# Optimization experiments

Hardware: AMD Instinct MI355X
Metric: run time of the kernel (lower is better)

Reference implementation:

```python
import jax, jax.numpy as jnp
import numpy as np

IN_DIMS = 1024
OUT_DIMS = 1024
N_TOKENS = 32768


def setup_inputs() -> dict:
    key = jax.random.key(0)
    k_x, k_wl0, k_wl1, k_scale, k_shift, k_noise = jax.random.split(key, 6)
    x = jax.random.normal(k_x, (N_TOKENS, IN_DIMS), dtype=jnp.float32)
    # weight_logits[..., 0]: magnitude logits, weight_logits[..., 1]: sign logits
    gain = np.sqrt(2.0)  # relu gain
    a = gain * np.sqrt(6.0 / (IN_DIMS + OUT_DIMS))
    mag_logits = jax.random.uniform(k_wl0, (OUT_DIMS, IN_DIMS), dtype=jnp.float32,
                                    minval=-a, maxval=a)  # logit(0.5)=0, so centered at 0
    sgn_logits = jax.random.uniform(k_wl1, (OUT_DIMS, IN_DIMS), dtype=jnp.float32,
                                    minval=-a, maxval=a)
    weight_logits = jnp.stack([mag_logits, sgn_logits], axis=-1)  # [O, I, 2]
    scale = jnp.full((OUT_DIMS,), np.float32(a), dtype=jnp.float32)
    shift = jnp.full((OUT_DIMS,), 0.01, dtype=jnp.float32)
    noise = jax.random.normal(k_noise, (N_TOKENS, OUT_DIMS), dtype=jnp.float32)
    return {"x": x, "weight_logits": weight_logits, "scale": scale,
            "shift": shift, "noise": noise}


def reference(x, weight_logits, scale, shift, noise):
    # train_forward of TernaryLinear
    weight_p = jax.nn.sigmoid(weight_logits)          # [O, I, 2]
    p_mag = weight_p[..., 0]                          # P(|w| = 1)
    p_sgn = weight_p[..., 1]                          # P(w > 0 | |w| = 1)
    s = 2.0 * p_sgn - 1.0
    weight_mean = p_mag * s                           # [O, I]
    weight_var = p_mag - (p_mag * p_mag) * (s * s)    # [O, I], >= 0
    out_mean = jnp.einsum('ni,oi->no', x, weight_mean)         # [N, O]
    out_var = jnp.einsum('ni,oi->no', x * x, weight_var)       # [N, O]
    out = out_mean + jnp.sqrt(out_var) * noise
    out = out * scale[None, :] + shift[None, :]
    return out
```

## Files before the change

### kernel.cpp

```cpp
#include <hip/hip_runtime.h>
#include <hip/hip_bf16.h>
#include <cmath>

#define N_TOK 32768
#define KDIM  1024
#define ODIM  1024

#define BM 128
#define BN 128
#define BK 64
#define NKT (KDIM / BK)
#define THREADS 512

typedef float          f32x4  __attribute__((ext_vector_type(4)));
typedef __bf16         bf16x8 __attribute__((ext_vector_type(8)));
typedef __bf16         bf16x4 __attribute__((ext_vector_type(4)));
typedef unsigned short us8    __attribute__((ext_vector_type(8)));
typedef unsigned short us2    __attribute__((ext_vector_type(2)));

static __device__ __forceinline__ unsigned short f2bf(float f) {
  unsigned u = __builtin_bit_cast(unsigned, f);
  u += 0x7FFFu + ((u >> 16) & 1u);
  return (unsigned short)(u >> 16);
}

static __device__ __forceinline__ f32x4 mfma16(us8 a, us8 b, f32x4 c) {
  return __builtin_amdgcn_mfma_f32_16x16x32_bf16(
      __builtin_bit_cast(bf16x8, a), __builtin_bit_cast(bf16x8, b), c, 0, 0, 0);
}

static __device__ __forceinline__ void gl_lds16(const void* g, void* l) {
  __builtin_amdgcn_global_load_lds(
      (const __attribute__((address_space(1))) void*)g,
      (__attribute__((address_space(3))) void*)l, 16, 0, 0);
}

__global__ void wprep_kernel(const float* __restrict__ wl,
                             unsigned short* __restrict__ wm,
                             unsigned short* __restrict__ wv) {
  int i = blockIdx.x * blockDim.x + threadIdx.x;
  f32x4 v = *reinterpret_cast<const f32x4*>(wl + (size_t)i * 4);
  float pm0 = 1.f / (1.f + expf(-v.x));
  float ps0 = 1.f / (1.f + expf(-v.y));
  float pm1 = 1.f / (1.f + expf(-v.z));
  float ps1 = 1.f / (1.f + expf(-v.w));
  float m0 = pm0 * (2.f * ps0 - 1.f);
  float m1 = pm1 * (2.f * ps1 - 1.f);
  float q0 = pm0 - m0 * m0;
  float q1 = pm1 - m1 * m1;
  us2 am = {f2bf(m0), f2bf(m1)};
  us2 av = {f2bf(q0), f2bf(q1)};
  *reinterpret_cast<us2*>(wm + (size_t)i * 2) = am;
  *reinterpret_cast<us2*>(wv + (size_t)i * 2) = av;
}

__global__ __launch_bounds__(THREADS, 4) void ternary_gemm(
    const float* __restrict__ x,
    const unsigned short* __restrict__ wm,
    const unsigned short* __restrict__ wv,
    const float* __restrict__ scale,
    const float* __restrict__ shift,
    const float* __restrict__ noise,
    float* __restrict__ out) {
  __shared__ alignas(16) char smem[67584];
  unsigned short* AsX  = (unsigned short*)smem;
  unsigned short* AsX2 = (unsigned short*)(smem + 16384);
  unsigned short* BsM  = (unsigned short*)(smem + 32768);
  unsigned short* BsV  = (unsigned short*)(smem + 49152);
  float* Mex = (float*)smem;
  float* Vex = ((float*)smem) + 4 * 32 * 66;

  const int tid  = threadIdx.x;
  const int lane = tid & 63;
  const int w    = tid >> 6;
  const bool isVar = (w >= 4);
  const int p    = w & 3;
  const int wr   = p >> 1;
  const int wc   = p & 1;
  const int l15  = lane & 15;
  const int l4   = lane >> 4;

  const int bid = blockIdx.x;
  const int swz = (bid & 7) * 256 + (bid >> 3);
  const int bm  = swz >> 3;
  const int bn  = swz & 7;
  const int rowBase = bm * BM;
  const int colBase = bn * BN;

  f32x4 acc[4][4];
#pragma unroll
  for (int i = 0; i < 4; ++i)
#pragma unroll
    for (int j = 0; j < 4; ++j) acc[i][j] = (f32x4)0.f;

  const float* xbase = x + (size_t)rowBase * KDIM;

  f32x4 apre[4];
#pragma unroll
  for (int jj = 0; jj < 4; ++jj) {
    int flat = jj * THREADS + tid;
    int r    = flat >> 4;
    int c4   = flat & 15;
    apre[jj] = *reinterpret_cast<const f32x4*>(xbase + (size_t)r * KDIM + c4 * 4);
  }

  const char* Abase = isVar ? (const char*)AsX2 : (const char*)AsX;
  const char* Bbase = isVar ? (const char*)BsV  : (const char*)BsM;

  for (int kt = 0; kt < NKT; ++kt) {
    const int k0 = kt * BK;

#pragma unroll
    for (int r = 0; r < 2; ++r) {
      int slot = r * THREADS + tid;
      int row  = slot >> 3;
      int j    = slot & 7;
      int ke   = (j ^ (row & 7)) << 3;
      size_t goff = (size_t)(colBase + row) * KDIM + k0 + ke;
      gl_lds16(wm + goff, (char*)BsM + slot * 16);
      gl_lds16(wv + goff, (char*)BsV + slot * 16);
    }

#pragma unroll
    for (int jj = 0; jj < 4; ++jj) {
      int flat = jj * THREADS + tid;
      int r    = flat >> 4;
      int c4   = flat & 15;
      f32x4 vx = apre[jj];
      bf16x4 bx  = {(__bf16)vx.x, (__bf16)vx.y, (__bf16)vx.z, (__bf16)vx.w};
      bf16x4 bx2 = {(__bf16)(vx.x * vx.x), (__bf16)(vx.y * vx.y),
                    (__bf16)(vx.z * vx.z), (__bf16)(vx.w * vx.w)};
      int off = r * 128 + ((c4 * 8) ^ ((r & 7) << 4));
      *reinterpret_cast<bf16x4*>((char*)AsX + off)  = bx;
      *reinterpret_cast<bf16x4*>((char*)AsX2 + off) = bx2;
    }

    __syncthreads();

    if (kt + 1 < NKT) {
      const float* xnext = xbase + (kt + 1) * BK;
#pragma unroll
      for (int jj = 0; jj < 4; ++jj) {
        int flat = jj * THREADS + tid;
        int r    = flat >> 4;
        int c4   = flat & 15;
        apre[jj] = *reinterpret_cast<const f32x4*>(xnext + (size_t)r * KDIM + c4 * 4);
      }
    }

#pragma unroll
    for (int ks = 0; ks < 2; ++ks) {
      us8 af[4], bf_[4];
      const int kb = ks * 64 + (l4 << 4);
#pragma unroll
      for (int am = 0; am < 4; ++am) {
        int row = wr * 64 + am * 16 + l15;
        int off = row * 128 + (kb ^ ((row & 7) << 4));
        af[am] = *reinterpret_cast<const us8*>(Abase + off);
      }
#pragma unroll
      for (int b = 0; b < 4; ++b) {
        int row = wc * 64 + b * 16 + l15;
        int off = row * 128 + (kb ^ ((row & 7) << 4));
        bf_[b] = *reinterpret_cast<const us8*>(Bbase + off);
      }
#pragma unroll
      for (int am = 0; am < 4; ++am)
#pragma unroll
        for (int b = 0; b < 4; ++b)
          acc[am][b] = mfma16(af[am], bf_[b], acc[am][b]);
    }
    __syncthreads();
  }

  if (!isVar) {
#pragma unroll
    for (int am = 2; am < 4; ++am)
#pragma unroll
      for (int b = 0; b < 4; ++b)
#pragma unroll
        for (int j = 0; j < 4; ++j) {
          int lr = am * 16 + l4 * 4 + j;
          int lc = b * 16 + l15;
          Mex[(p * 32 + (lr - 32)) * 66 + lc] = acc[am][b][j];
        }
  } else {
#pragma unroll
    for (int am = 0; am < 2; ++am)
#pragma unroll
      for (int b = 0; b < 4; ++b)
#pragma unroll
        for (int j = 0; j < 4; ++j) {
          int lr = am * 16 + l4 * 4 + j;
          int lc = b * 16 + l15;
          Vex[(p * 32 + lr) * 66 + lc] = acc[am][b][j];
        }
  }
  __syncthreads();

  if (!isVar) {
#pragma unroll
    for (int am = 0; am < 2; ++am)
#pragma unroll
      for (int b = 0; b < 4; ++b) {
        int col = colBase + wc * 64 + b * 16 + l15;
        float sc = scale[col];
        float sh = shift[col];
#pragma unroll
        for (int j = 0; j < 4; ++j) {
          int lr = am * 16 + l4 * 4 + j;
          float vv = Vex[(p * 32 + lr) * 66 + b * 16 + l15];
          size_t idx = (size_t)(rowBase + wr * 64 + lr) * ODIM + col;
          out[idx] = fmaf(acc[am][b][j] + sqrtf(fmaxf(vv, 0.f)) * noise[idx], sc, sh);
        }
      }
  } else {
#pragma unroll
    for (int am = 2; am < 4; ++am)
#pragma unroll
      for (int b = 0; b < 4; ++b) {
        int col = colBase + wc * 64 + b * 16 + l15;
        float sc = scale[col];
        float sh = shift[col];
#pragma unroll
        for (int j = 0; j < 4; ++j) {
          int lr = am * 16 + l4 * 4 + j;
          float mm = Mex[(p * 32 + (lr - 32)) * 66 + b * 16 + l15];
          size_t idx = (size_t)(rowBase + wr * 64 + lr) * ODIM + col;
          out[idx] = fmaf(mm + sqrtf(fmaxf(acc[am][b][j], 0.f)) * noise[idx], sc, sh);
        }
      }
  }
}

extern "C" void kernel_launch(void* const* d_in, const int* in_sizes, int n_in,
                              void* d_out, int out_size, void* d_ws, size_t ws_size,
                              hipStream_t stream) {
  const float* x     = (const float*)d_in[0];
  const float* wl    = (const float*)d_in[1];
  const float* scale = (const float*)d_in[2];
  const float* shift = (const float*)d_in[3];
  const float* noise = (const float*)d_in[4];
  float* out = (float*)d_out;

  unsigned short* wm = (unsigned short*)d_ws;
  unsigned short* wv = wm + (size_t)ODIM * KDIM;

  wprep_kernel<<<(ODIM * KDIM / 2) / 256, 256, 0, stream>>>(wl, wm, wv);

  ternary_gemm<<<(N_TOK / BM) * (ODIM / BN), THREADS, 0, stream>>>(
      x, wm, wv, scale, shift, noise, out);
}
```

Baseline: 207.9 us.

## Double-buffer LDS, enlarge row tile to 256, square x on the fly per warp

Moves the GEMM to a 256x128 tile with double-buffered LDS stages. The next k-tile's weight and x loads are issued before the current tile's MFMAs, and the bf16 x tile is written into the next buffer after compute, so only one barrier is needed per k-step. x is stored once in bf16, and the variance warps square it after reading it from LDS, instead of a second x² buffer being kept. This uses 128KB of LDS with occupancy 2, 128 accumulators per thread and extra ALU work in the variance warps, and it changes the epilogue exchange layout to an XOR swizzle.

```diff
diff --git a/kernel.cpp b/kernel.cpp
--- a/kernel.cpp
+++ b/kernel.cpp
@@ -6,17 +6,17 @@
 #define KDIM  1024
 #define ODIM  1024
 
-#define BM 128
+#define BM 256
 #define BN 128
 #define BK 64
 #define NKT (KDIM / BK)
 #define THREADS 512
+#define BUFSZ 65536
 
 typedef float          f32x4  __attribute__((ext_vector_type(4)));
 typedef __bf16         bf16x8 __attribute__((ext_vector_type(8)));
-typedef __bf16         bf16x4 __attribute__((ext_vector_type(4)));
 typedef unsigned short us8    __attribute__((ext_vector_type(8)));
-typedef unsigned short us2    __attribute__((ext_vector_type(2)));
+typedef unsigned short us2   __attribute__((ext_vector_type(2)));
 
 static __device__ __forceinline__ unsigned short f2bf(float f) {
   unsigned u = __builtin_bit_cast(unsigned, f);
@@ -24,6 +24,10 @@
   return (unsigned short)(u >> 16);
 }
 
+static __device__ __forceinline__ unsigned short bfc(float f) {
+  return __builtin_bit_cast(unsigned short, (__bf16)f);
+}
+
 static __device__ __forceinline__ f32x4 mfma16(us8 a, us8 b, f32x4 c) {
   return __builtin_amdgcn_mfma_f32_16x16x32_bf16(
       __builtin_bit_cast(bf16x8, a), __builtin_bit_cast(bf16x8, b), c, 0, 0, 0);
@@ -33,6 +37,16 @@
   __builtin_amdgcn_global_load_lds(
       (const __attribute__((address_space(1))) void*)g,
       (__attribute__((address_space(3))) void*)l, 16, 0, 0);
+}
+
+static __device__ __forceinline__ us8 sqr8(us8 a) {
+  us8 r;
+#pragma unroll
+  for (int i = 0; i < 8; ++i) {
+    float f = __builtin_bit_cast(float, (unsigned)a[i] << 16);
+    r[i] = bfc(f * f);
+  }
+  return r;
 }
 
 __global__ void wprep_kernel(const float* __restrict__ wl,
@@ -54,7 +68,7 @@
   *reinterpret_cast<us2*>(wv + (size_t)i * 2) = av;
 }
 
-__global__ __launch_bounds__(THREADS, 4) void ternary_gemm(
+__global__ __launch_bounds__(THREADS, 2) void ternary_gemm(
     const float* __restrict__ x,
     const unsigned short* __restrict__ wm,
     const unsigned short* __restrict__ wv,
@@ -62,13 +76,7 @@
     const float* __restrict__ shift,
     const float* __restrict__ noise,
     float* __restrict__ out) {
-  __shared__ alignas(16) char smem[67584];
-  unsigned short* AsX  = (unsigned short*)smem;
-  unsigned short* AsX2 = (unsigned short*)(smem + 16384);
-  unsigned short* BsM  = (unsigned short*)(smem + 32768);
-  unsigned short* BsV  = (unsigned short*)(smem + 49152);
-  float* Mex = (float*)smem;
-  float* Vex = ((float*)smem) + 4 * 32 * 66;
+  __shared__ alignas(16) char smem[2 * BUFSZ];
 
   const int tid  = threadIdx.x;
   const int lane = tid & 63;
@@ -81,153 +89,156 @@
   const int l4   = lane >> 4;
 
   const int bid = blockIdx.x;
-  const int swz = (bid & 7) * 256 + (bid >> 3);
+  const int swz = (bid & 7) * 128 + (bid >> 3);
   const int bm  = swz >> 3;
   const int bn  = swz & 7;
   const int rowBase = bm * BM;
   const int colBase = bn * BN;
 
-  f32x4 acc[4][4];
-#pragma unroll
-  for (int i = 0; i < 4; ++i)
+  f32x4 acc[8][4];
+#pragma unroll
+  for (int i = 0; i < 8; ++i)
 #pragma unroll
     for (int j = 0; j < 4; ++j) acc[i][j] = (f32x4)0.f;
 
-  const float* xbase = x + (size_t)rowBase * KDIM;
-
-  f32x4 apre[4];
-#pragma unroll
-  for (int jj = 0; jj < 4; ++jj) {
-    int flat = jj * THREADS + tid;
-    int r    = flat >> 4;
-    int c4   = flat & 15;
-    apre[jj] = *reinterpret_cast<const f32x4*>(xbase + (size_t)r * KDIM + c4 * 4);
-  }
-
-  const char* Abase = isVar ? (const char*)AsX2 : (const char*)AsX;
-  const char* Bbase = isVar ? (const char*)BsV  : (const char*)BsM;
+  const float* xb = x + (size_t)rowBase * KDIM;
+
+  auto stageB = [&](int kt, char* buf) {
+    const int k0 = kt * BK;
+    char* BsM = buf + 32768;
+    char* BsV = buf + 49152;
+#pragma unroll
+    for (int c = 0; c < 2; ++c) {
+      int flat = c * THREADS + tid;
+      int row  = flat >> 3;
+      int j    = flat & 7;
+      size_t goff = (size_t)(colBase + row) * KDIM + k0 + ((j ^ (row & 7)) << 3);
+      gl_lds16(wm + goff, BsM + flat * 16);
+      gl_lds16(wv + goff, BsV + flat * 16);
+    }
+  };
+  auto loadX = [&](int kt, f32x4* ap) {
+    const float* xt = xb + kt * BK;
+#pragma unroll
+    for (int c = 0; c < 4; ++c) {
+      int flat = c * THREADS + tid;
+      int row  = flat >> 3;
+      int j    = flat & 7;
+      const float* s = xt + (size_t)row * KDIM + j * 8;
+      ap[2 * c]     = *reinterpret_cast<const f32x4*>(s);
+      ap[2 * c + 1] = *reinterpret_cast<const f32x4*>(s + 4);
+    }
+  };
+  auto writeA = [&](const f32x4* ap, char* buf) {
+#pragma unroll
+    for (int c = 0; c < 4; ++c) {
+      int flat = c * THREADS + tid;
+      int row  = flat >> 3;
+      int j    = flat & 7;
+      f32x4 v0 = ap[2 * c], v1 = ap[2 * c + 1];
+      us8 o = {bfc(v0.x), bfc(v0.y), bfc(v0.z), bfc(v0.w),
+               bfc(v1.x), bfc(v1.y), bfc(v1.z), bfc(v1.w)};
+      int off = row * 128 + ((j * 16) ^ ((row & 7) << 4));
+      *reinterpret_cast<us8*>(buf + off) = o;
+    }
+  };
+
+  f32x4 ap[8];
+  stageB(0, smem);
+  loadX(0, ap);
+  writeA(ap, smem);
+  __syncthreads();
 
   for (int kt = 0; kt < NKT; ++kt) {
-    const int k0 = kt * BK;
-
-#pragma unroll
-    for (int r = 0; r < 2; ++r) {
-      int slot = r * THREADS + tid;
-      int row  = slot >> 3;
-      int j    = slot & 7;
-      int ke   = (j ^ (row & 7)) << 3;
-      size_t goff = (size_t)(colBase + row) * KDIM + k0 + ke;
-      gl_lds16(wm + goff, (char*)BsM + slot * 16);
-      gl_lds16(wv + goff, (char*)BsV + slot * 16);
-    }
-
-#pragma unroll
-    for (int jj = 0; jj < 4; ++jj) {
-      int flat = jj * THREADS + tid;
-      int r    = flat >> 4;
-      int c4   = flat & 15;
-      f32x4 vx = apre[jj];
-      bf16x4 bx  = {(__bf16)vx.x, (__bf16)vx.y, (__bf16)vx.z, (__bf16)vx.w};
-      bf16x4 bx2 = {(__bf16)(vx.x * vx.x), (__bf16)(vx.y * vx.y),
-                    (__bf16)(vx.z * vx.z), (__bf16)(vx.w * vx.w)};
-      int off = r * 128 + ((c4 * 8) ^ ((r & 7) << 4));
-      *reinterpret_cast<bf16x4*>((char*)AsX + off)  = bx;
-      *reinterpret_cast<bf16x4*>((char*)AsX2 + off) = bx2;
-    }
-
-    __syncthreads();
-
-    if (kt + 1 < NKT) {
-      const float* xnext = xbase + (kt + 1) * BK;
-#pragma unroll
-      for (int jj = 0; jj < 4; ++jj) {
-        int flat = jj * THREADS + tid;
-        int r    = flat >> 4;
-        int c4   = flat & 15;
-        apre[jj] = *reinterpret_cast<const f32x4*>(xnext + (size_t)r * KDIM + c4 * 4);
-      }
-    }
-
+    const char* cur = smem + (size_t)(kt & 1) * BUFSZ;
+    char*       nxt = smem + (size_t)((kt + 1) & 1) * BUFSZ;
+
+    if (kt + 1 < NKT) { stageB(kt + 1, nxt); loadX(kt + 1, ap); }
+
+    const char* Ab = cur;
+    const char* Bb = cur + 32768 + (isVar ? 16384 : 0);
 #pragma unroll
     for (int ks = 0; ks < 2; ++ks) {
-      us8 af[4], bf_[4];
       const int kb = ks * 64 + (l4 << 4);
-#pragma unroll
-      for (int am = 0; am < 4; ++am) {
-        int row = wr * 64 + am * 16 + l15;
-        int off = row * 128 + (kb ^ ((row & 7) << 4));
-        af[am] = *reinterpret_cast<const us8*>(Abase + off);
-      }
+      us8 bf_[4], af[8];
 #pragma unroll
       for (int b = 0; b < 4; ++b) {
         int row = wc * 64 + b * 16 + l15;
-        int off = row * 128 + (kb ^ ((row & 7) << 4));
-        bf_[b] = *reinterpret_cast<const us8*>(Bbase + off);
-      }
-#pragma unroll
-      for (int am = 0; am < 4; ++am)
+        bf_[b] = *reinterpret_cast<const us8*>(Bb + row * 128 + (kb ^ ((row & 7) << 4)));
+      }
+#pragma unroll
+      for (int i = 0; i < 8; ++i) {
+        int row = wr * 128 + i * 16 + l15;
+        af[i] = *reinterpret_cast<const us8*>(Ab + row * 128 + (kb ^ ((row & 7) << 4)));
+        if (isVar) af[i] = sqr8(af[i]);
+      }
+#pragma unroll
+      for (int i = 0; i < 8; ++i)
 #pragma unroll
         for (int b = 0; b < 4; ++b)
-          acc[am][b] = mfma16(af[am], bf_[b], acc[am][b]);
-    }
+          acc[i][b] = mfma16(af[i], bf_[b], acc[i][b]);
+    }
+
+    if (kt + 1 < NKT) writeA(ap, nxt);
+
     __syncthreads();
   }
 
+  float* Mx = (float*)smem;
+  float* Vx = (float*)(smem + 65536);
   if (!isVar) {
 #pragma unroll
-    for (int am = 2; am < 4; ++am)
+    for (int i = 4; i < 8; ++i)
 #pragma unroll
       for (int b = 0; b < 4; ++b)
 #pragma unroll
         for (int j = 0; j < 4; ++j) {
-          int lr = am * 16 + l4 * 4 + j;
+          int lr = (i - 4) * 16 + l4 * 4 + j;
           int lc = b * 16 + l15;
-          Mex[(p * 32 + (lr - 32)) * 66 + lc] = acc[am][b][j];
+          Mx[(p * 64 + lr) * 64 + (lc ^ ((lr & 4) << 2))] = acc[i][b][j];
         }
   } else {
 #pragma unroll
-    for (int am = 0; am < 2; ++am)
+    for (int i = 0; i < 4; ++i)
 #pragma unroll
       for (int b = 0; b < 4; ++b)
 #pragma unroll
         for (int j = 0; j < 4; ++j) {
-          int lr = am * 16 + l4 * 4 + j;
+          int lr = i * 16 + l4 * 4 + j;
           int lc = b * 16 + l15;
-          Vex[(p * 32 + lr) * 66 + lc] = acc[am][b][j];
+          Vx[(p * 64 + lr) * 64 + (lc ^ ((lr & 4) << 2))] = acc[i][b][j];
         }
   }
   __syncthreads();
 
   if (!isVar) {
 #pragma unroll
-    for (int am = 0; am < 2; ++am)
+    for (int i = 0; i < 4; ++i)
 #pragma unroll
       for (int b = 0; b < 4; ++b) {
         int col = colBase + wc * 64 + b * 16 + l15;
-        float sc = scale[col];
-        float sh = shift[col];
-#pragma unroll
-        for (int j = 0; j < 4; ++j) {
-          int lr = am * 16 + l4 * 4 + j;
-          float vv = Vex[(p * 32 + lr) * 66 + b * 16 + l15];
-          size_t idx = (size_t)(rowBase + wr * 64 + lr) * ODIM + col;
-          out[idx] = fmaf(acc[am][b][j] + sqrtf(fmaxf(vv, 0.f)) * noise[idx], sc, sh);
+        float sc = scale[col], sh = shift[col];
+#pragma unroll
+        for (int j = 0; j < 4; ++j) {
+          int lr = i * 16 + l4 * 4 + j;
+          float vv = Vx[(p * 64 + lr) * 64 + ((b * 16 + l15) ^ ((lr & 4) << 2))];
+          size_t idx = (size_t)(rowBase + wr * 128 + lr) * ODIM + col;
+          out[idx] = fmaf(acc[i][b][j] + sqrtf(fmaxf(vv, 0.f)) * noise[idx], sc, sh);
         }
       }
   } else {
 #pragma unroll
-    for (int am = 2; am < 4; ++am)
+    for (int i = 4; i < 8; ++i)
 #pragma unroll
       for (int b = 0; b < 4; ++b) {
         int col = colBase + wc * 64 + b * 16 + l15;
-        float sc = scale[col];
-        float sh = shift[col];
-#pragma unroll
-        for (int j = 0; j < 4; ++j) {
-          int lr = am * 16 + l4 * 4 + j;
-          float mm = Mex[(p * 32 + (lr - 32)) * 66 + b * 16 + l15];
-          size_t idx = (size_t)(rowBase + wr * 64 + lr) * ODIM + col;
-          out[idx] = fmaf(mm + sqrtf(fmaxf(acc[am][b][j], 0.f)) * noise[idx], sc, sh);
+        float sc = scale[col], sh = shift[col];
+#pragma unroll
+        for (int j = 0; j < 4; ++j) {
+          int lr = (i - 4) * 16 + l4 * 4 + j;
+          float mm = Mx[(p * 64 + lr) * 64 + ((b * 16 + l15) ^ ((lr & 4) << 2))];
+          size_t idx = (size_t)(rowBase + wr * 128 + 64 + lr) * ODIM + col;
+          out[idx] = fmaf(mm + sqrtf(fmaxf(acc[i][b][j], 0.f)) * noise[idx], sc, sh);
         }
       }
   }
```

Result: slower. 252.0 us (+21.2%).
